# Performance work log

Measured on AMD Instinct MI355X. Metric: run time of the kernel, lower is better.

Reference implementation:

```python
import jax, jax.numpy as jnp
import numpy as np

WIN, SIGMA = 11, 1.5
C1, C2, EPS = 0.01 ** 2, 0.03 ** 2, 1e-8


def _gauss_window(win=WIN, sigma=SIGMA):
    coords = jnp.arange(win, dtype=jnp.float32) - (win - 1) / 2
    g = jnp.exp(-coords ** 2 / (2 * sigma ** 2))
    g = g / g.sum()
    return (g[:, None] * g[None, :])[None, None, :, :]


def setup_inputs() -> dict:
    key = jax.random.key(0)
    k1, k2 = jax.random.split(key)
    N, C, H, W = 32, 1, 512, 512
    x = jax.random.uniform(k1, (N, C, H, W), dtype=jnp.float32)
    y = jax.random.uniform(k2, (N, C, H, W), dtype=jnp.float32)
    w = _gauss_window()
    return {"x": x, "y": y, "w": w}


def _conv(x, w):
    pad = w.shape[-1] // 2
    return jax.lax.conv_general_dilated(
        x, w, window_strides=(1, 1), padding=[(pad, pad), (pad, pad)],
        dimension_numbers=("NCHW", "OIHW", "NCHW"))


def reference(x, y, w):
    w = w.astype(x.dtype)
    n = x.shape[0]
    # One fused conv over all five planes stacked on the batch dim.
    stacked = jnp.concatenate([x, y, x * x, y * y, x * y], axis=0)
    conv = _conv(stacked, w)
    mu_x, mu_y, ex2, ey2, exy = (conv[i * n:(i + 1) * n] for i in range(5))
    mu_x2, mu_y2, mu_xy = mu_x ** 2, mu_y ** 2, mu_x * mu_y
    sig_x2 = ex2 - mu_x2
    sig_y2 = ey2 - mu_y2
    sig_xy = exy - mu_xy
    num = (2 * mu_xy + C1) * (2 * sig_xy + C2)
    den = (mu_x2 + mu_y2 + C1) * (sig_x2 + sig_y2 + C2)
    return jnp.clip(num / (den + EPS), 0.0, 1.0).mean()
```

## Files before the change

### kernel.cpp

```cpp
#include <hip/hip_runtime.h>


typedef float v2f __attribute__((ext_vector_type(2)));
typedef float v4f __attribute__((ext_vector_type(4)));

#define IMG_H 512
#define IMG_W 512
#define NIMG  32
#define NT    256
#define RROWS 23
#define ITERS (RROWS + 10)
#define SEGW  144

#define C1F  1.0e-4f
#define C2F  9.0e-4f
#define EPSF 1.0e-8f

static __device__ __forceinline__ v2f pkfma(float s, v2f a, v2f b) {
    v2f sv = {s, s};
    return __builtin_elementwise_fma(sv, a, b);
}

__global__ __launch_bounds__(NT) void ssim_kernel(
    const float* __restrict__ xg, const float* __restrict__ yg,
    const float* __restrict__ wg, float* __restrict__ out)
{
    const int t    = threadIdx.x;
    const int lane = t & 63;
    const int wv   = t >> 6;
    const int chnk = blockIdx.x;
    const int img  = blockIdx.y;
    const int r0   = chnk * RROWS;
    const int C0   = 128 * wv;
    const int cown = C0 + 2 * lane;
    const int c0l  = 2 * lane;

    const float* xb = xg + (size_t)img * (IMG_H * IMG_W);
    const float* yb = yg + (size_t)img * (IMG_H * IMG_W);

    __shared__ alignas(16) v2f seg[4][SEGW];
    __shared__ float wredS[4];

    float rs = 0.f;
    if (lane < 11) {
        #pragma unroll
        for (int j = 0; j < 11; ++j) rs += wg[lane * 11 + j];
    }
    float g[11];
    #pragma unroll
    for (int k = 0; k < 11; ++k) {
        int gi = __shfl(__float_as_int(rs), k, 64);
        g[k] = __int_as_float(__builtin_amdgcn_readfirstlane(gi));
    }

    const v2f z2 = {0.f, 0.f};

    const bool isH = (lane < 3) || (lane >= 61);
    const int  hcol = (lane < 3) ? (C0 - 6 + 2 * lane)
                                 : (C0 + 128 + 2 * (lane - 61));
    const int  hidx = (lane < 3) ? (2 * lane) : (134 + 2 * (lane - 61));

    v2f px, py, hx, hy;
    {
        const int r = r0 - 5;
        px = z2; py = z2; hx = z2; hy = z2;
        if ((unsigned)r < IMG_H) {
            const float* xr = xb + (size_t)r * IMG_W;
            const float* yr = yb + (size_t)r * IMG_W;
            px = *(const v2f*)(xr + cown);
            py = *(const v2f*)(yr + cown);
            if (isH && (unsigned)hcol < IMG_W) {
                hx = *(const v2f*)(xr + hcol);
                hy = *(const v2f*)(yr + hcol);
            }
        }
    }

    v2f rSD[11][2], rQ[11][2];

    float acc = 0.f;

    #pragma unroll 1
    for (int base = 0; base < ITERS; base += 11) {
        #pragma unroll
        for (int s = 0; s < 11; ++s) {
            const int i = base + s;

            {
                const v2f sv = px + py;
                const v2f dv = px - py;
                v4f st = {sv.x, dv.x, sv.y, dv.y};
                *(v4f*)&seg[wv][6 + c0l] = st;
                if (isH) {
                    const v2f hs = hx + hy;
                    const v2f hd = hx - hy;
                    v4f ht = {hs.x, hd.x, hs.y, hd.y};
                    *(v4f*)&seg[wv][hidx] = ht;
                }
            }

            if (i < ITERS - 1) {
                const int r = r0 - 4 + i;
                px = z2; py = z2; hx = z2; hy = z2;
                if ((unsigned)r < IMG_H) {
                    const float* xr = xb + (size_t)r * IMG_W;
                    const float* yr = yb + (size_t)r * IMG_W;
                    px = *(const v2f*)(xr + cown);
                    py = *(const v2f*)(yr + cown);
                    if (isH && (unsigned)hcol < IMG_W) {
                        hx = *(const v2f*)(xr + hcol);
                        hy = *(const v2f*)(yr + hcol);
                    }
                }
            }

            v2f hA = z2, hB = z2, qA = z2, qB = z2;
            #pragma unroll
            for (int m = 0; m < 7; ++m) {
                const v4f w4 = *(const v4f*)&seg[wv][c0l + 2 * m];
                const v2f e0 = {w4.x, w4.y};
                const v2f e1 = {w4.z, w4.w};
                {
                    const int j = 2 * m;
                    if (j >= 1) {
                        const v2f f0 = e0 * e0;
                        if (j <= 11) {
                            hA = pkfma(g[j - 1], e0, hA);
                            qA = pkfma(g[j - 1], f0, qA);
                        }
                        if (j >= 2) {
                            hB = pkfma(g[j - 2], e0, hB);
                            qB = pkfma(g[j - 2], f0, qB);
                        }
                    }
                }
                {
                    const int j = 2 * m + 1;
                    if (j <= 12) {
                        const v2f f1 = e1 * e1;
                        if (j <= 11) {
                            hA = pkfma(g[j - 1], e1, hA);
                            qA = pkfma(g[j - 1], f1, qA);
                        }
                        if (j >= 2) {
                            hB = pkfma(g[j - 2], e1, hB);
                            qB = pkfma(g[j - 2], f1, qB);
                        }
                    }
                }
            }
            rSD[s][0] = hA; rSD[s][1] = hB;
            rQ[s][0]  = qA; rQ[s][1]  = qB;

            if (i >= 10) {
                const int orow = r0 + i - 10;
                if (orow < IMG_H) {
                    #pragma unroll
                    for (int cc = 0; cc < 2; ++cc) {
                        v2f mSD = z2, mQ = z2;
                        #pragma unroll
                        for (int j = 0; j < 11; ++j) {
                            const int sl = (s + 1 + j) % 11;
                            mSD = pkfma(g[j], rSD[sl][cc], mSD);
                            mQ  = pkfma(g[j], rQ[sl][cc],  mQ);
                        }
                        const v2f t2 = mSD * mSD;
                        const float a    = 0.5f  * (t2.x + t2.y);
                        const float muxy = 0.25f * (t2.x - t2.y);
                        const float ep   = 0.5f  * (mQ.x + mQ.y);
                        const float eq   = 0.25f * (mQ.x - mQ.y);
                        const float sxy  = eq - muxy;
                        const float ssum = ep - a;
                        const float num  = fmaf(2.f, muxy, C1F) * fmaf(2.f, sxy, C2F);
                        const float den  = (a + C1F) * (ssum + C2F);
                        float v = num * __builtin_amdgcn_rcpf(den + EPSF);
                        acc += fminf(fmaxf(v, 0.f), 1.f);
                    }
                }
            }
        }
    }

    #pragma unroll
    for (int off = 32; off > 0; off >>= 1)
        acc += __shfl_down(acc, off, 64);
    if (lane == 0) wredS[wv] = acc;
    __syncthreads();
    if (t == 0) {
        const float tot = (wredS[0] + wredS[1]) + (wredS[2] + wredS[3]);
        atomicAdd(out, tot * (1.0f / (float)((size_t)NIMG * IMG_H * IMG_W)));
    }
}

extern "C" void kernel_launch(void* const* d_in, const int* in_sizes, int n_in,
                              void* d_out, int out_size, void* d_ws, size_t ws_size,
                              hipStream_t stream) {
    const float* x = (const float*)d_in[0];
    const float* y = (const float*)d_in[1];
    const float* w = (const float*)d_in[2];
    float* out = (float*)d_out;

    hipMemsetAsync(out, 0, sizeof(float), stream);

    dim3 grid((IMG_H + RROWS - 1) / RROWS, NIMG);
    ssim_kernel<<<grid, dim3(NT), 0, stream>>>(x, y, w, out);
}
```

Before: 117.2 us.

## Triple-buffer LDS row segments and prefetch rows two ahead

Replaces the single per-wave LDS row buffer with a 3-slot ring. Each row's LDS reads are issued before the next row's write, and global loads are prefetched two rows ahead to hide load and LDS latency. The register ring of horizontal results grows from 11 to 12 so its length divides the new 36-iteration loop, which is unrolled by 12. Rows per block rise from 23 to 26, cutting the grid to 20 chunks per image and reducing halo overhead, at the cost of more registers and fewer blocks.

```diff
diff --git a/kernel.cpp b/kernel.cpp
--- a/kernel.cpp
+++ b/kernel.cpp
@@ -8,8 +8,9 @@
 #define IMG_W 512
 #define NIMG  32
 #define NT    256
-#define RROWS 23
-#define ITERS (RROWS + 10)
+#define RROWS 26
+#define NCHX  20
+#define ITERS 36
 #define SEGW  144
 
 #define C1F  1.0e-4f
@@ -38,7 +39,7 @@
     const float* xb = xg + (size_t)img * (IMG_H * IMG_W);
     const float* yb = yg + (size_t)img * (IMG_H * IMG_W);
 
-    __shared__ alignas(16) v2f seg[4][SEGW];
+    __shared__ alignas(16) v2f seg[4][3][SEGW];
     __shared__ float wredS[4];
 
     float rs = 0.f;
@@ -61,63 +62,64 @@
     const int  hidx = (lane < 3) ? (2 * lane) : (134 + 2 * (lane - 61));
 
     v2f px, py, hx, hy;
-    {
-        const int r = r0 - 5;
-        px = z2; py = z2; hx = z2; hy = z2;
-        if ((unsigned)r < IMG_H) {
-            const float* xr = xb + (size_t)r * IMG_W;
-            const float* yr = yb + (size_t)r * IMG_W;
-            px = *(const v2f*)(xr + cown);
-            py = *(const v2f*)(yr + cown);
-            if (isH && (unsigned)hcol < IMG_W) {
-                hx = *(const v2f*)(xr + hcol);
-                hy = *(const v2f*)(yr + hcol);
-            }
-        }
-    }
-
-    v2f rSD[11][2], rQ[11][2];
+
+#define LOADROW(ROW) do {                                                  \
+        const int r_ = (ROW);                                              \
+        px = z2; py = z2; hx = z2; hy = z2;                                \
+        if ((unsigned)r_ < IMG_H) {                                        \
+            const float* xr = xb + (size_t)r_ * IMG_W;                     \
+            const float* yr = yb + (size_t)r_ * IMG_W;                     \
+            px = *(const v2f*)(xr + cown);                                 \
+            py = *(const v2f*)(yr + cown);                                 \
+            if (isH && (unsigned)hcol < IMG_W) {                           \
+                hx = *(const v2f*)(xr + hcol);                             \
+                hy = *(const v2f*)(yr + hcol);                             \
+            }                                                              \
+        }                                                                  \
+    } while (0)
+
+#define WRITESLOT(SL) do {                                                 \
+        const v2f sv_ = px + py;                         \
+        const v2f dv_ = px - py;                                           \
+        v4f st_ = {sv_.x, dv_.x, sv_.y, dv_.y};                            \
+        *(v4f*)&seg[wv][(SL)][6 + c0l] = st_;                              \
+        if (isH) {                                                         \
+            const v2f hs_ = hx + hy;                                       \
+            const v2f hd_ = hx - hy;                                       \
+            v4f ht_ = {hs_.x, hd_.x, hs_.y, hd_.y};                        \
+            *(v4f*)&seg[wv][(SL)][hidx] = ht_;                             \
+        }                                                                  \
+    } while (0)
+
+    LOADROW(r0 - 5);
+    WRITESLOT(0);
+    LOADROW(r0 - 4);
+    WRITESLOT(1);
+    LOADROW(r0 - 3);
+
+    v2f rSD[12][2], rQ[12][2];
 
     float acc = 0.f;
 
     #pragma unroll 1
-    for (int base = 0; base < ITERS; base += 11) {
+    for (int base = 0; base < ITERS; base += 12) {
         #pragma unroll
-        for (int s = 0; s < 11; ++s) {
+        for (int s = 0; s < 12; ++s) {
             const int i = base + s;
 
-            {
-                const v2f sv = px + py;
-                const v2f dv = px - py;
-                v4f st = {sv.x, dv.x, sv.y, dv.y};
-                *(v4f*)&seg[wv][6 + c0l] = st;
-                if (isH) {
-                    const v2f hs = hx + hy;
-                    const v2f hd = hx - hy;
-                    v4f ht = {hs.x, hd.x, hs.y, hd.y};
-                    *(v4f*)&seg[wv][hidx] = ht;
-                }
-            }
-
-            if (i < ITERS - 1) {
-                const int r = r0 - 4 + i;
-                px = z2; py = z2; hx = z2; hy = z2;
-                if ((unsigned)r < IMG_H) {
-                    const float* xr = xb + (size_t)r * IMG_W;
-                    const float* yr = yb + (size_t)r * IMG_W;
-                    px = *(const v2f*)(xr + cown);
-                    py = *(const v2f*)(yr + cown);
-                    if (isH && (unsigned)hcol < IMG_W) {
-                        hx = *(const v2f*)(xr + hcol);
-                        hy = *(const v2f*)(yr + hcol);
-                    }
-                }
-            }
+            v4f w4r[7];
+            #pragma unroll
+            for (int m = 0; m < 7; ++m)
+                w4r[m] = *(const v4f*)&seg[wv][s % 3][c0l + 2 * m];
+
+            WRITESLOT((s + 2) % 3);
+
+            LOADROW(r0 - 5 + i + 3);
 
             v2f hA = z2, hB = z2, qA = z2, qB = z2;
             #pragma unroll
             for (int m = 0; m < 7; ++m) {
-                const v4f w4 = *(const v4f*)&seg[wv][c0l + 2 * m];
+                const v4f w4 = w4r[m];
                 const v2f e0 = {w4.x, w4.y};
                 const v2f e1 = {w4.z, w4.w};
                 {
@@ -160,7 +162,7 @@
                         v2f mSD = z2, mQ = z2;
                         #pragma unroll
                         for (int j = 0; j < 11; ++j) {
-                            const int sl = (s + 1 + j) % 11;
+                            const int sl = (s + 2 + j) % 12;
                             mSD = pkfma(g[j], rSD[sl][cc], mSD);
                             mQ  = pkfma(g[j], rQ[sl][cc],  mQ);
                         }
@@ -202,6 +204,6 @@
 
     hipMemsetAsync(out, 0, sizeof(float), stream);
 
-    dim3 grid((IMG_H + RROWS - 1) / RROWS, NIMG);
+    dim3 grid(NCHX, NIMG);
     ssim_kernel<<<grid, dim3(NT), 0, stream>>>(x, y, w, out);
 }
```

New measurement: 120.8 us. +3.0%, slower.
